# Optimization experiments

Measured on AMD Instinct MI355X. Metric: run time of the kernel, lower is better.

Reference implementation:

```python
import jax, jax.numpy as jnp
import numpy as np


def _conv(x, w, b, pad):
    y = jax.lax.conv_general_dilated(x, w, (1, 1), [(pad, pad), (pad, pad)],
                                     dimension_numbers=('NCHW', 'OIHW', 'NCHW'))
    return y + b[None, :, None, None]


def _leaky(x):
    return jnp.where(x >= 0, x, 0.2 * x)


def _up_nearest(t, s):
    return jnp.repeat(jnp.repeat(t, s, axis=2), s, axis=3)


def _to_plane(d, dx, dy, size):
    # nearest-upsample d,dx,dy by `size` and add per-subpixel plane offsets
    c = jnp.linspace(-(size - 1) / 2, (size - 1) / 2, size).astype(d.dtype)
    H, W = d.shape[2], d.shape[3]
    a = jnp.tile(c, W)[None, None, None, :]   # x-offset pattern along width
    b = jnp.tile(c, H)[None, None, :, None]   # y-offset pattern along height
    return _up_nearest(d, size) + a * _up_nearest(dx, size) + b * _up_nearest(dy, size)


def _warp(x, disp):
    # grid_sample(x, grid) with grid = (xx - disp, yy), align_corners=True, zero padding.
    # y coords are exact integers, so this reduces to 1-D linear interp along W.
    B, C, H, W = x.shape
    ix = jnp.arange(W, dtype=x.dtype)[None, None, :] - disp[:, 0]  # [B,H,W]
    x0 = jnp.floor(ix)
    wx = ix - x0
    x0i = x0.astype(jnp.int32)
    x1i = x0i + 1
    ok0 = ((x0i >= 0) & (x0i < W)).astype(x.dtype)
    ok1 = ((x1i >= 0) & (x1i < W)).astype(x.dtype)

    def gather(idx):
        idx = jnp.clip(idx, 0, W - 1)
        return jnp.take_along_axis(x, jnp.broadcast_to(idx[:, None], (B, C, H, W)), axis=3)

    return ((1 - wx) * ok0)[:, None] * gather(x0i) + (wx * ok1)[:, None] * gather(x1i)


def _unshuffle(x, r=4):
    B, C, H, W = x.shape
    return x.reshape(B, C, H // r, r, W // r, r).transpose(0, 1, 3, 5, 2, 4).reshape(B, C * r * r, H // r, W // r)


def _tile_warping(tile_plane, fea_l, fea_r):
    d, dx, dy = tile_plane[:, 0:1], tile_plane[:, 1:2], tile_plane[:, 2:3]
    cvs = []
    for k in (-1.0, 0.0, 1.0):
        local_d = _to_plane(d + k, dx, dy, 4)
        cv = jnp.sum(jnp.abs(fea_l - _warp(fea_r, local_d)), axis=1, keepdims=True)
        cvs.append(_unshuffle(cv, 4))
    return jnp.concatenate(cvs, axis=1)


def _upsample_hyp(h, scale=2.0, size=2):
    d = _to_plane(h[:, 0:1], h[:, 1:2], h[:, 2:3], size) * scale
    rest = _up_nearest(h[:, 1:], size)
    return jnp.concatenate([d, rest], axis=1)


def _forward(fea_l, fea_r, cur, prev,
             w_dec, b_dec, w0, b0,
             w_r0c1, b_r0c1, w_r0c2, b_r0c2,
             w_r1c1, b_r1c1, w_r1c2, b_r1c2,
             w_last, b_last):
    fea = _unshuffle(jnp.sum(jnp.abs(fea_l), axis=1, keepdims=True), 4)  # [B,16,H/4,W/4]

    cur_cv = _tile_warping(cur[:, :3], fea_l, fea_r)
    cur_cv = _leaky(_conv(jnp.concatenate([fea, cur_cv], 1), w_dec, b_dec, 0))

    up_prev = _upsample_hyp(prev, 2.0, 2)
    prev_cv = _tile_warping(up_prev[:, :3], fea_l, fea_r)
    prev_cv = _leaky(_conv(jnp.concatenate([fea, prev_cv], 1), w_dec, b_dec, 0))

    aug = jnp.concatenate([cur, cur_cv, up_prev, prev_cv], 1)  # 64 ch
    h = _leaky(_conv(aug, w0, b0, 0))
    # resblock0 (BasicBlock + outer LeakyReLU)
    t = _leaky(_conv(h, w_r0c1, b_r0c1, 1))
    h = _leaky(_conv(t, w_r0c2, b_r0c2, 1) + h)
    # resblock1
    t = _leaky(_conv(h, w_r1c1, b_r1c1, 1))
    h = _leaky(_conv(t, w_r1c2, b_r1c2, 1) + h)
    u = _conv(h, w_last, b_last, 1)  # 34 ch

    conf = u[:, :2]
    prev_delta = u[:, 2:18]
    cur_delta = u[:, 18:34]
    mask = jnp.argmax(conf, axis=1, keepdims=True).astype(u.dtype)

    upd_cur = cur + cur_delta
    upd_cur = jnp.concatenate([jax.nn.relu(upd_cur[:, :1]), upd_cur[:, 1:]], 1)
    upd_prev = up_prev + prev_delta
    upd_prev = jnp.concatenate([jax.nn.relu(upd_prev[:, :1]), upd_prev[:, 1:]], 1)

    refined = mask * upd_cur + (1 - mask) * upd_prev
    return (refined,
            jnp.concatenate([upd_cur, conf[:, 1:2]], 1),
            jnp.concatenate([upd_prev, conf[:, :1]], 1))


def setup_inputs() -> dict:
    key = jax.random.key(0)
    ks = jax.random.split(key, 16)
    B, C, H, W = 2, 16, 384, 1280
    Ht, Wt = H // 4, W // 4
    inp = {
        'fea_l': jax.random.normal(ks[0], (B, C, H, W), jnp.float32),
        'fea_r': jax.random.normal(ks[1], (B, C, H, W), jnp.float32),
        'current_hypothesis': jax.random.uniform(ks[2], (B, 16, Ht, Wt), jnp.float32) * 4.0,
        'prev_hypothesis': jax.random.uniform(ks[3], (B, 16, Ht // 2, Wt // 2), jnp.float32) * 4.0,
    }
    s = 0.05
    inp['w_dec'] = jax.random.normal(ks[4], (16, 64, 1, 1), jnp.float32) * s
    inp['b_dec'] = jax.random.normal(ks[5], (16,), jnp.float32) * s
    inp['w0'] = jax.random.normal(ks[6], (32, 64, 1, 1), jnp.float32) * s
    inp['b0'] = jax.random.normal(ks[7], (32,), jnp.float32) * s
    inp['w_r0c1'] = jax.random.normal(ks[8], (32, 32, 3, 3), jnp.float32) * s
    inp['b_r0c1'] = jax.random.normal(ks[9], (32,), jnp.float32) * s
    inp['w_r0c2'] = jax.random.normal(ks[10], (32, 32, 3, 3), jnp.float32) * s
    inp['b_r0c2'] = jax.random.normal(ks[11], (32,), jnp.float32) * s
    inp['w_r1c1'] = jax.random.normal(ks[12], (32, 32, 3, 3), jnp.float32) * s
    inp['b_r1c1'] = jax.random.normal(ks[13], (32,), jnp.float32) * s
    inp['w_r1c2'] = jax.random.normal(ks[14], (32, 32, 3, 3), jnp.float32) * s
    inp['b_r1c2'] = jax.random.normal(ks[15], (32,), jnp.float32) * s
    k2 = jax.random.split(jax.random.key(1), 2)
    inp['w_last'] = jax.random.normal(k2[0], (34, 32, 3, 3), jnp.float32) * s
    inp['b_last'] = jax.random.normal(k2[1], (34,), jnp.float32) * s
    return inp


def reference(fea_l, fea_r, current_hypothesis, prev_hypothesis,
              w_dec, b_dec, w0, b0,
              w_r0c1, b_r0c1, w_r0c2, b_r0c2,
              w_r1c1, b_r1c1, w_r1c2, b_r1c2,
              w_last, b_last):
    return _forward(fea_l, fea_r, current_hypothesis, prev_hypothesis,
                    w_dec, b_dec, w0, b0,
                    w_r0c1, b_r0c1, w_r0c2, b_r0c2,
                    w_r1c1, b_r1c1, w_r1c2, b_r1c2,
                    w_last, b_last)
```

## Files before the change

kernel.cpp:

```cpp
#include <hip/hip_runtime.h>
#include <hip/hip_bf16.h>

#define B_ 2
#define C_ 16
#define H_ 384
#define W_ 1280
#define HT_ 96
#define WT_ 320
#define SP_ (HT_*WT_)
#define NPIX_ (B_*SP_)
#define HP_ 48
#define WP_ 160
#define SPP_ (HP_*WP_)

__device__ __forceinline__ float leaky(float v){ return v >= 0.f ? v : 0.2f*v; }

__global__ __launch_bounds__(256) void k_sentinel(float* __restrict__ out, int n, float v){
    int i = blockIdx.x*256 + threadIdx.x;
    if (i < n) out[i] = v;
}

template <bool PREV>
__global__ __launch_bounds__(256) void k_warpdec(const float* __restrict__ plane,
        const float* __restrict__ fl, const float* __restrict__ fr,
        const float* __restrict__ wdec, const float* __restrict__ bdec,
        float* __restrict__ outcv){
    __shared__ float vals[16][65];
    __shared__ float wl[64][16];
    int tid = threadIdx.x;
    for (int i = tid; i < 1024; i += 256) wl[i>>4][i&15] = wdec[(i&15)*64 + (i>>4)];

    int tp  = tid >> 4;
    int sub = tid & 15;
    int yy = sub >> 2, xx = sub & 3;
    int ty = blockIdx.y;
    int tx = blockIdx.x*16 + tp;
    int b  = blockIdx.z;
    int y = ty*4 + yy, x = tx*4 + xx;

    float d, dxv, dyv;
    if (PREV){
        size_t pb = ((size_t)(b*16)*HP_ + (ty>>1))*WP_ + (tx>>1);
        float pd  = plane[pb];
        float pdx = plane[pb + SPP_];
        float pdy = plane[pb + 2*SPP_];
        float cx = (tx & 1) ? 0.5f : -0.5f;
        float cy = (ty & 1) ? 0.5f : -0.5f;
        d   = (pd + cx*pdx + cy*pdy) * 2.0f;
        dxv = pdx;
        dyv = pdy;
    } else {
        size_t pb = ((size_t)(b*16)*HT_ + ty)*WT_ + tx;
        d   = plane[pb];
        dxv = plane[pb + SP_];
        dyv = plane[pb + 2*SP_];
    }
    const float c4[4] = {-1.5f,-0.5f,0.5f,1.5f};
    float ld0 = d + c4[xx]*dxv + c4[yy]*dyv;
    float ix  = (float)x - ld0;
    float x0f = floorf(ix);
    float wx  = ix - x0f;
    int   x0  = (int)x0f;
    float wlo[4], whi[4]; int xc[4];
    #pragma unroll
    for (int j = 0; j < 4; j++){
        int xi = x0 + (j-1);
        bool ok = (xi >= 0) && (xi < W_);
        xc[j]  = xi < 0 ? 0 : (xi > W_-1 ? W_-1 : xi);
        wlo[j] = ok ? (1.f - wx) : 0.f;
        whi[j] = ok ? wx : 0.f;
    }
    const float* pl = fl + (size_t)(b*C_)*H_*W_ + (size_t)y*W_ + x;
    const float* pr = fr + (size_t)(b*C_)*H_*W_ + (size_t)y*W_;
    float fsum=0.f, s0=0.f, s1=0.f, s2=0.f;
    #pragma unroll 4
    for (int c = 0; c < C_; c++){
        float a = pl[(size_t)c*H_*W_];
        const float* prc = pr + (size_t)c*H_*W_;
        float v0 = prc[xc[0]];
        float v1 = prc[xc[1]];
        float v2 = prc[xc[2]];
        float v3 = prc[xc[3]];
        fsum += fabsf(a);
        s0 += fabsf(a - (wlo[2]*v2 + whi[3]*v3));
        s1 += fabsf(a - (wlo[1]*v1 + whi[2]*v2));
        s2 += fabsf(a - (wlo[0]*v0 + whi[1]*v1));
    }
    vals[tp][sub]      = fsum;
    vals[tp][16 + sub] = s0;
    vals[tp][32 + sub] = s1;
    vals[tp][48 + sub] = s2;
    __syncthreads();
    int oc  = tid >> 4;
    int tp2 = tid & 15;
    float acc = bdec[oc];
    #pragma unroll 8
    for (int ic = 0; ic < 64; ic++) acc += vals[tp2][ic] * wl[ic][oc];
    outcv[((size_t)(b*16 + oc)*HT_ + ty)*WT_ + blockIdx.x*16 + tp2] = leaky(acc);
}

__global__ __launch_bounds__(256) void k_conv0(const float* __restrict__ cur,
        const float* __restrict__ ccv, const float* __restrict__ prev,
        const float* __restrict__ pcv, const float* __restrict__ w,
        const float* __restrict__ bias, float* __restrict__ out){
    __shared__ float wl[64][32];
    __shared__ float bl[32];
    int tid = threadIdx.x;
    for (int i = tid; i < 2048; i += 256) wl[i>>5][i&31] = w[(i&31)*64 + (i>>5)];
    if (tid < 32) bl[tid] = bias[tid];
    __syncthreads();
    int idx = blockIdx.x*256 + tid;
    int b = idx / SP_, sp = idx % SP_;
    int y = sp / WT_, x = sp % WT_;
    float acc[32];
    #pragma unroll
    for (int o = 0; o < 32; o++) acc[o] = 0.f;
    const float* p0 = cur + (size_t)b*16*SP_ + sp;
    #pragma unroll 2
    for (int i = 0; i < 16; i++){
        float v = p0[(size_t)i*SP_];
        #pragma unroll
        for (int o = 0; o < 32; o++) acc[o] += v*wl[i][o];
    }
    const float* p1 = ccv + (size_t)b*16*SP_ + sp;
    #pragma unroll 2
    for (int i = 0; i < 16; i++){
        float v = p1[(size_t)i*SP_];
        #pragma unroll
        for (int o = 0; o < 32; o++) acc[o] += v*wl[16+i][o];
    }
    size_t src = ((size_t)(b*16)*HP_ + (y>>1))*WP_ + (x>>1);
    {
        float pd  = prev[src];
        float pdx = prev[src + SPP_];
        float pdy = prev[src + 2*SPP_];
        float cx = (x & 1) ? 0.5f : -0.5f;
        float cy = (y & 1) ? 0.5f : -0.5f;
        float v = (pd + cx*pdx + cy*pdy) * 2.0f;
        #pragma unroll
        for (int o = 0; o < 32; o++) acc[o] += v*wl[32][o];
    }
    #pragma unroll 2
    for (int i = 1; i < 16; i++){
        float v = prev[src + (size_t)i*SPP_];
        #pragma unroll
        for (int o = 0; o < 32; o++) acc[o] += v*wl[32+i][o];
    }
    const float* p3 = pcv + (size_t)b*16*SP_ + sp;
    #pragma unroll 2
    for (int i = 0; i < 16; i++){
        float v = p3[(size_t)i*SP_];
        #pragma unroll
        for (int o = 0; o < 32; o++) acc[o] += v*wl[48+i][o];
    }
    float* po = out + (size_t)b*32*SP_ + sp;
    #pragma unroll
    for (int o = 0; o < 32; o++) po[(size_t)o*SP_] = leaky(acc[o] + bl[o]);
}

template<bool RES>
__global__ __launch_bounds__(256) void k_conv3(const float* __restrict__ in,
        const float* __restrict__ w, const float* __restrict__ bias,
        const float* res, float* out){
    __shared__ float it[8][6][34];
    __shared__ float wl[8][9][32];
    int tid = threadIdx.x;
    int gx = blockIdx.x*32, gy = blockIdx.y*4;
    int b = blockIdx.z;
    int ocg  = tid >> 5;
    int slot = tid & 31;
    int tx4  = (slot & 7)*4;
    int ty   = slot >> 3;
    float acc[4][4];
    #pragma unroll
    for (int o = 0; o < 4; o++)
        #pragma unroll
        for (int p = 0; p < 4; p++) acc[o][p] = 0.f;

    for (int ic0 = 0; ic0 < 32; ic0 += 8){
        for (int i = tid; i < 8*6*34; i += 256){
            int ic = i/(6*34); int r = i - ic*(6*34);
            int iy = r/34;     int ixx = r - iy*34;
            int ggy = gy + iy - 1, ggx = gx + ixx - 1;
            float v = 0.f;
            if (ggy >= 0 && ggy < HT_ && ggx >= 0 && ggx < WT_)
                v = in[((size_t)(b*32 + ic0+ic)*HT_ + ggy)*WT_ + ggx];
            it[ic][iy][ixx] = v;
        }
        for (int i = tid; i < 2304; i += 256){
            int ic = i/288; int r = i - ic*288;
            int kk = r >> 5; int oc = r & 31;
            wl[ic][kk][oc] = w[(size_t)(oc*32 + ic0+ic)*9 + kk];
        }
        __syncthreads();
        #pragma unroll
        for (int ic = 0; ic < 8; ic++){
            #pragma unroll
            for (int dy = 0; dy < 3; dy++){
                float inr[6];
                #pragma unroll
                for (int j = 0; j < 6; j++) inr[j] = it[ic][ty+dy][tx4+j];
                #pragma unroll
                for (int dx = 0; dx < 3; dx++){
                    const float4 wv = *(const float4*)(&wl[ic][dy*3+dx][ocg*4]);
                    const float wa[4] = {wv.x, wv.y, wv.z, wv.w};
                    #pragma unroll
                    for (int o = 0; o < 4; o++)
                        #pragma unroll
                        for (int p = 0; p < 4; p++)
                            acc[o][p] += inr[dx+p]*wa[o];
                }
            }
        }
        __syncthreads();
    }
    int oc0 = ocg*4;
    int yo = gy + ty;
    #pragma unroll
    for (int o = 0; o < 4; o++){
        float bo = bias[oc0+o];
        size_t ob = ((size_t)(b*32 + oc0+o)*HT_ + yo)*WT_ + gx + tx4;
        #pragma unroll
        for (int p = 0; p < 4; p++){
            float v = acc[o][p] + bo;
            if (RES) v += res[ob+p];
            out[ob+p] = leaky(v);
        }
    }
}

__global__ __launch_bounds__(256) void k_last(const float* __restrict__ in,
        const float* __restrict__ w, const float* __restrict__ bias,
        const float* __restrict__ cur, const float* __restrict__ prev,
        float* __restrict__ out){
    __shared__ float it[8][10][34];
    __shared__ float wl[8][9][36];
    __shared__ float bl[34];
    int tid = threadIdx.x;
    int gx = blockIdx.x*32, gy = blockIdx.y*8;
    int b = blockIdx.z;
    int tx = tid & 31, ty = tid >> 5;
    if (tid < 34) bl[tid] = bias[tid];
    float acc[34];
    #pragma unroll
    for (int o = 0; o < 34; o++) acc[o] = 0.f;

    for (int ic0 = 0; ic0 < 32; ic0 += 8){
        for (int i = tid; i < 8*10*34; i += 256){
            int ic = i/340; int r = i - ic*340;
            int iy = r/34;  int ixx = r - iy*34;
            int ggy = gy + iy - 1, ggx = gx + ixx - 1;
            float v = 0.f;
            if (ggy >= 0 && ggy < HT_ && ggx >= 0 && ggx < WT_)
                v = in[((size_t)(b*32 + ic0+ic)*HT_ + ggy)*WT_ + ggx];
            it[ic][iy][ixx] = v;
        }
        for (int i = tid; i < 8*9*34; i += 256){
            int ic = i/306; int r = i - ic*306;
            int kk = r/34;  int oc = r - kk*34;
            wl[ic][kk][oc] = w[(size_t)(oc*32 + ic0+ic)*9 + kk];
        }
        __syncthreads();
        for (int ic = 0; ic < 8; ic++){
            #pragma unroll
            for (int dy = 0; dy < 3; dy++){
                const float vv[3] = { it[ic][ty+dy][tx], it[ic][ty+dy][tx+1], it[ic][ty+dy][tx+2] };
                #pragma unroll
                for (int dx = 0; dx < 3; dx++){
                    const float* wp = &wl[ic][dy*3+dx][0];
                    float v = vv[dx];
                    #pragma unroll
                    for (int o = 0; o < 34; o++) acc[o] += v*wp[o];
                }
            }
        }
        __syncthreads();
    }
    int x = gx + tx, y = gy + ty;
    size_t pix = (size_t)y*WT_ + x;
    float conf0 = acc[0] + bl[0];
    float conf1 = acc[1] + bl[1];
    bool m = conf1 > conf0;
    size_t src = ((size_t)(b*16)*HP_ + (y>>1))*WP_ + (x>>1);
    float cx = (x & 1) ? 0.5f : -0.5f;
    float cy = (y & 1) ? 0.5f : -0.5f;
    const float* cp = cur + (size_t)b*16*SP_ + pix;
    float* o0 = out +               (size_t)b*16*SP_ + pix;
    float* o1 = out +  983040u  +   (size_t)b*17*SP_ + pix;
    float* o2 = out + 2027520u  +   (size_t)b*17*SP_ + pix;
    #pragma unroll
    for (int c = 0; c < 16; c++){
        float upv;
        if (c == 0){
            float dv  = prev[src];
            float dxv = prev[src + SPP_];
            float dyv = prev[src + 2*SPP_];
            upv = (dv + cx*dxv + cy*dyv) * 2.0f;
        } else {
            upv = prev[src + (size_t)c*SPP_];
        }
        float ucv = cp[(size_t)c*SP_] + acc[18+c] + bl[18+c];
        upv = upv + acc[2+c] + bl[2+c];
        if (c == 0){ ucv = fmaxf(ucv, 0.f); upv = fmaxf(upv, 0.f); }
        float rf = m ? ucv : upv;
        o0[(size_t)c*SP_] = rf;
        o1[(size_t)c*SP_] = ucv;
        o2[(size_t)c*SP_] = upv;
    }
    o1[(size_t)16*SP_] = conf1;
    o2[(size_t)16*SP_] = conf0;
}

#define WS_NEED (32u*NPIX_*4u)
#define OUT_ELEMS 3072000

extern "C" void kernel_launch(void* const* d_in, const int* in_sizes, int n_in,
                              void* d_out, int out_size, void* d_ws, size_t ws_size,
                              hipStream_t stream) {
    const float* fea_l  = (const float*)d_in[0];
    const float* fea_r  = (const float*)d_in[1];
    const float* cur    = (const float*)d_in[2];
    const float* prev   = (const float*)d_in[3];
    const float* w_dec  = (const float*)d_in[4];
    const float* b_dec  = (const float*)d_in[5];
    const float* w0     = (const float*)d_in[6];
    const float* b0     = (const float*)d_in[7];
    const float* w_r0c1 = (const float*)d_in[8];
    const float* b_r0c1 = (const float*)d_in[9];
    const float* w_r0c2 = (const float*)d_in[10];
    const float* b_r0c2 = (const float*)d_in[11];
    const float* w_r1c1 = (const float*)d_in[12];
    const float* b_r1c1 = (const float*)d_in[13];
    const float* w_r1c2 = (const float*)d_in[14];
    const float* b_r1c2 = (const float*)d_in[15];
    const float* w_last = (const float*)d_in[16];
    const float* b_last = (const float*)d_in[17];

    float* out = (float*)d_out;

    if (ws_size < (size_t)WS_NEED){
        k_sentinel<<<(OUT_ELEMS+255)/256, 256, 0, stream>>>(out, OUT_ELEMS, (float)(ws_size >> 10));
        return;
    }

    float* h = (float*)d_ws;
    float* curcv  = out;
    float* prevcv = out + 983040;
    float* t      = out;

    dim3 gw(20, 96, 2);
    k_warpdec<false><<<gw, 256, 0, stream>>>(cur,  fea_l, fea_r, w_dec, b_dec, curcv);
    k_warpdec<true> <<<gw, 256, 0, stream>>>(prev, fea_l, fea_r, w_dec, b_dec, prevcv);

    k_conv0<<<240, 256, 0, stream>>>(cur, curcv, prev, prevcv, w0, b0, h);

    dim3 g3(10, 24, 2);
    k_conv3<false><<<g3, 256, 0, stream>>>(h, w_r0c1, b_r0c1, nullptr, t);
    k_conv3<true> <<<g3, 256, 0, stream>>>(t, w_r0c2, b_r0c2, h, h);
    k_conv3<false><<<g3, 256, 0, stream>>>(h, w_r1c1, b_r1c1, nullptr, t);
    k_conv3<true> <<<g3, 256, 0, stream>>>(t, w_r1c2, b_r1c2, h, h);

    dim3 gl(10, 12, 2);
    k_last<<<gl, 256, 0, stream>>>(h, w_last, b_last, cur, prev, out);
}
```

Measured before the change: 492.4 us.

## Fuse warp cost volumes and 1x1 conv0 into one front kernel; retile last conv

The two warp+decoder kernels and the 1x1 conv0 become a single kernel. It computes the current and previous cost volumes together, sharing the fea_l loads and the fsum term, and applies conv0 from shared memory, so the intermediate cost volumes never go through global memory. The last 3x3 conv now uses the same register-blocked 4x4 tiling as k_conv3 with extra output channels, staging results in shared memory for the epilogue. The conv3 shared tile is padded to 36 for float4/float2 vectorized reads. The cost is more shared memory and registers per block in the fused kernel, and only half of the threads run the epilogue in k_last.

```diff
diff --git a/kernel.cpp b/kernel.cpp
--- a/kernel.cpp
+++ b/kernel.cpp
@@ -20,149 +20,174 @@
     if (i < n) out[i] = v;
 }
 
-template <bool PREV>
-__global__ __launch_bounds__(256) void k_warpdec(const float* __restrict__ plane,
+__global__ __launch_bounds__(256) void k_front(
+        const float* __restrict__ cur, const float* __restrict__ prev,
         const float* __restrict__ fl, const float* __restrict__ fr,
         const float* __restrict__ wdec, const float* __restrict__ bdec,
-        float* __restrict__ outcv){
-    __shared__ float vals[16][65];
-    __shared__ float wl[64][16];
+        const float* __restrict__ w0, const float* __restrict__ b0,
+        float* __restrict__ h){
+    __shared__ float wdl[64][17];
+    __shared__ float w0l[64][33];
+    __shared__ float pl6[16][6];
+    __shared__ float vals[16][117];
+    __shared__ float cvl[16][33];
+    __shared__ float cul[16][33];
     int tid = threadIdx.x;
-    for (int i = tid; i < 1024; i += 256) wl[i>>4][i&15] = wdec[(i&15)*64 + (i>>4)];
-
-    int tp  = tid >> 4;
-    int sub = tid & 15;
-    int yy = sub >> 2, xx = sub & 3;
-    int ty = blockIdx.y;
-    int tx = blockIdx.x*16 + tp;
-    int b  = blockIdx.z;
-    int y = ty*4 + yy, x = tx*4 + xx;
-
-    float d, dxv, dyv;
-    if (PREV){
-        size_t pb = ((size_t)(b*16)*HP_ + (ty>>1))*WP_ + (tx>>1);
-        float pd  = plane[pb];
-        float pdx = plane[pb + SPP_];
-        float pdy = plane[pb + 2*SPP_];
+    int ty = blockIdx.y, b = blockIdx.z;
+    int tx0 = blockIdx.x*16;
+
+    for (int i = tid; i < 1024; i += 256) wdl[i>>4][i&15] = wdec[(i&15)*64 + (i>>4)];
+    for (int i = tid; i < 2048; i += 256) w0l[i>>5][i&31] = w0[(i&31)*64 + (i>>5)];
+    if (tid < 16){
+        int tx = tx0 + tid;
+        size_t pb = ((size_t)(b*16)*HT_ + ty)*WT_ + tx;
+        pl6[tid][0] = cur[pb];
+        pl6[tid][1] = cur[pb + SP_];
+        pl6[tid][2] = cur[pb + 2*SP_];
+        size_t qb = ((size_t)(b*16)*HP_ + (ty>>1))*WP_ + (tx>>1);
+        float pd  = prev[qb];
+        float pdx = prev[qb + SPP_];
+        float pdy = prev[qb + 2*SPP_];
         float cx = (tx & 1) ? 0.5f : -0.5f;
         float cy = (ty & 1) ? 0.5f : -0.5f;
-        d   = (pd + cx*pdx + cy*pdy) * 2.0f;
-        dxv = pdx;
-        dyv = pdy;
-    } else {
-        size_t pb = ((size_t)(b*16)*HT_ + ty)*WT_ + tx;
-        d   = plane[pb];
-        dxv = plane[pb + SP_];
-        dyv = plane[pb + 2*SP_];
-    }
+        pl6[tid][3] = (pd + cx*pdx + cy*pdy) * 2.0f;
+        pl6[tid][4] = pdx;
+        pl6[tid][5] = pdy;
+    }
+    {
+        int i = tid >> 4, px = tid & 15;
+        int tx = tx0 + px;
+        cul[px][i] = cur[(size_t)(b*16 + i)*SP_ + (size_t)ty*WT_ + tx];
+        float upv;
+        if (i == 0) upv = 0.f;
+        else upv = prev[(size_t)(b*16 + i)*SPP_ + (size_t)(ty>>1)*WP_ + (tx>>1)];
+        cul[px][16 + i] = upv;
+    }
+    __syncthreads();
+    if (tid < 16) cul[tid][16] = pl6[tid][3];
+
+    int r  = tid >> 6;
+    int cx = tid & 63;
+    int tp = cx >> 2, xx = cx & 3, yy = r;
+    int x = tx0*4 + cx, y = ty*4 + r;
+    int sub = yy*4 + xx;
+
+    float dC = pl6[tp][0], dxC = pl6[tp][1], dyC = pl6[tp][2];
+    float dP = pl6[tp][3], dxP = pl6[tp][4], dyP = pl6[tp][5];
     const float c4[4] = {-1.5f,-0.5f,0.5f,1.5f};
-    float ld0 = d + c4[xx]*dxv + c4[yy]*dyv;
-    float ix  = (float)x - ld0;
-    float x0f = floorf(ix);
-    float wx  = ix - x0f;
-    int   x0  = (int)x0f;
-    float wlo[4], whi[4]; int xc[4];
-    #pragma unroll
-    for (int j = 0; j < 4; j++){
-        int xi = x0 + (j-1);
-        bool ok = (xi >= 0) && (xi < W_);
-        xc[j]  = xi < 0 ? 0 : (xi > W_-1 ? W_-1 : xi);
-        wlo[j] = ok ? (1.f - wx) : 0.f;
-        whi[j] = ok ? wx : 0.f;
+    float ldC = dC + c4[xx]*dxC + c4[yy]*dyC;
+    float ldP = dP + c4[xx]*dxP + c4[yy]*dyP;
+
+    float wloC[4], whiC[4], wloP[4], whiP[4];
+    int xcC[4], xcP[4];
+    {
+        float ix  = (float)x - ldC;
+        float x0f = floorf(ix);
+        float wx  = ix - x0f;
+        int x0 = (int)x0f;
+        #pragma unroll
+        for (int j = 0; j < 4; j++){
+            int xi = x0 + (j-1);
+            bool ok = (xi >= 0) && (xi < W_);
+            xcC[j]  = xi < 0 ? 0 : (xi > W_-1 ? W_-1 : xi);
+            wloC[j] = ok ? (1.f - wx) : 0.f;
+            whiC[j] = ok ? wx : 0.f;
+        }
+        ix  = (float)x - ldP;
+        x0f = floorf(ix);
+        wx  = ix - x0f;
+        x0 = (int)x0f;
+        #pragma unroll
+        for (int j = 0; j < 4; j++){
+            int xi = x0 + (j-1);
+            bool ok = (xi >= 0) && (xi < W_);
+            xcP[j]  = xi < 0 ? 0 : (xi > W_-1 ? W_-1 : xi);
+            wloP[j] = ok ? (1.f - wx) : 0.f;
+            whiP[j] = ok ? wx : 0.f;
+        }
     }
     const float* pl = fl + (size_t)(b*C_)*H_*W_ + (size_t)y*W_ + x;
     const float* pr = fr + (size_t)(b*C_)*H_*W_ + (size_t)y*W_;
-    float fsum=0.f, s0=0.f, s1=0.f, s2=0.f;
-    #pragma unroll 4
+    float fsum=0.f, c0=0.f, c1=0.f, c2=0.f, p0=0.f, p1=0.f, p2=0.f;
+    #pragma unroll 8
     for (int c = 0; c < C_; c++){
         float a = pl[(size_t)c*H_*W_];
         const float* prc = pr + (size_t)c*H_*W_;
-        float v0 = prc[xc[0]];
-        float v1 = prc[xc[1]];
-        float v2 = prc[xc[2]];
-        float v3 = prc[xc[3]];
+        float uC0 = prc[xcC[0]], uC1 = prc[xcC[1]], uC2 = prc[xcC[2]], uC3 = prc[xcC[3]];
+        float uP0 = prc[xcP[0]], uP1 = prc[xcP[1]], uP2 = prc[xcP[2]], uP3 = prc[xcP[3]];
         fsum += fabsf(a);
-        s0 += fabsf(a - (wlo[2]*v2 + whi[3]*v3));
-        s1 += fabsf(a - (wlo[1]*v1 + whi[2]*v2));
-        s2 += fabsf(a - (wlo[0]*v0 + whi[1]*v1));
+        c0 += fabsf(a - (wloC[2]*uC2 + whiC[3]*uC3));
+        c1 += fabsf(a - (wloC[1]*uC1 + whiC[2]*uC2));
+        c2 += fabsf(a - (wloC[0]*uC0 + whiC[1]*uC1));
+        p0 += fabsf(a - (wloP[2]*uP2 + whiP[3]*uP3));
+        p1 += fabsf(a - (wloP[1]*uP1 + whiP[2]*uP2));
+        p2 += fabsf(a - (wloP[0]*uP0 + whiP[1]*uP1));
     }
     vals[tp][sub]      = fsum;
-    vals[tp][16 + sub] = s0;
-    vals[tp][32 + sub] = s1;
-    vals[tp][48 + sub] = s2;
+    vals[tp][16+sub]   = c0;
+    vals[tp][32+sub]   = c1;
+    vals[tp][48+sub]   = c2;
+    vals[tp][64+sub]   = p0;
+    vals[tp][80+sub]   = p1;
+    vals[tp][96+sub]   = p2;
     __syncthreads();
-    int oc  = tid >> 4;
-    int tp2 = tid & 15;
-    float acc = bdec[oc];
-    #pragma unroll 8
-    for (int ic = 0; ic < 64; ic++) acc += vals[tp2][ic] * wl[ic][oc];
-    outcv[((size_t)(b*16 + oc)*HT_ + ty)*WT_ + blockIdx.x*16 + tp2] = leaky(acc);
-}
-
-__global__ __launch_bounds__(256) void k_conv0(const float* __restrict__ cur,
-        const float* __restrict__ ccv, const float* __restrict__ prev,
-        const float* __restrict__ pcv, const float* __restrict__ w,
-        const float* __restrict__ bias, float* __restrict__ out){
-    __shared__ float wl[64][32];
-    __shared__ float bl[32];
-    int tid = threadIdx.x;
-    for (int i = tid; i < 2048; i += 256) wl[i>>5][i&31] = w[(i&31)*64 + (i>>5)];
-    if (tid < 32) bl[tid] = bias[tid];
+
+    {
+        int oc = tid >> 4, px = tid & 15;
+        float bb = bdec[oc];
+        float accC = bb, accP = bb;
+        #pragma unroll 8
+        for (int ic = 0; ic < 16; ic++){
+            float wv = wdl[ic][oc];
+            accC += vals[px][ic] * wv;
+            accP += vals[px][ic] * wv;
+        }
+        #pragma unroll 8
+        for (int ic = 16; ic < 64; ic++){
+            float wv = wdl[ic][oc];
+            accC += vals[px][ic]      * wv;
+            accP += vals[px][ic + 48] * wv;
+        }
+        cvl[px][oc]      = leaky(accC);
+        cvl[px][16 + oc] = leaky(accP);
+    }
     __syncthreads();
-    int idx = blockIdx.x*256 + tid;
-    int b = idx / SP_, sp = idx % SP_;
-    int y = sp / WT_, x = sp % WT_;
-    float acc[32];
-    #pragma unroll
-    for (int o = 0; o < 32; o++) acc[o] = 0.f;
-    const float* p0 = cur + (size_t)b*16*SP_ + sp;
-    #pragma unroll 2
-    for (int i = 0; i < 16; i++){
-        float v = p0[(size_t)i*SP_];
-        #pragma unroll
-        for (int o = 0; o < 32; o++) acc[o] += v*wl[i][o];
-    }
-    const float* p1 = ccv + (size_t)b*16*SP_ + sp;
-    #pragma unroll 2
-    for (int i = 0; i < 16; i++){
-        float v = p1[(size_t)i*SP_];
-        #pragma unroll
-        for (int o = 0; o < 32; o++) acc[o] += v*wl[16+i][o];
-    }
-    size_t src = ((size_t)(b*16)*HP_ + (y>>1))*WP_ + (x>>1);
+
     {
-        float pd  = prev[src];
-        float pdx = prev[src + SPP_];
-        float pdy = prev[src + 2*SPP_];
-        float cx = (x & 1) ? 0.5f : -0.5f;
-        float cy = (y & 1) ? 0.5f : -0.5f;
-        float v = (pd + cx*pdx + cy*pdy) * 2.0f;
-        #pragma unroll
-        for (int o = 0; o < 32; o++) acc[o] += v*wl[32][o];
-    }
-    #pragma unroll 2
-    for (int i = 1; i < 16; i++){
-        float v = prev[src + (size_t)i*SPP_];
-        #pragma unroll
-        for (int o = 0; o < 32; o++) acc[o] += v*wl[32+i][o];
-    }
-    const float* p3 = pcv + (size_t)b*16*SP_ + sp;
-    #pragma unroll 2
-    for (int i = 0; i < 16; i++){
-        float v = p3[(size_t)i*SP_];
-        #pragma unroll
-        for (int o = 0; o < 32; o++) acc[o] += v*wl[48+i][o];
-    }
-    float* po = out + (size_t)b*32*SP_ + sp;
-    #pragma unroll
-    for (int o = 0; o < 32; o++) po[(size_t)o*SP_] = leaky(acc[o] + bl[o]);
+        int pair = tid >> 4, px = tid & 15;
+        int oc0 = pair*2;
+        float a0 = b0[oc0], a1 = b0[oc0+1];
+        #pragma unroll 4
+        for (int i = 0; i < 16; i++){
+            float v = cul[px][i];
+            a0 += v*w0l[i][oc0]; a1 += v*w0l[i][oc0+1];
+        }
+        #pragma unroll 4
+        for (int i = 0; i < 16; i++){
+            float v = cvl[px][i];
+            a0 += v*w0l[16+i][oc0]; a1 += v*w0l[16+i][oc0+1];
+        }
+        #pragma unroll 4
+        for (int i = 0; i < 16; i++){
+            float v = cul[px][16+i];
+            a0 += v*w0l[32+i][oc0]; a1 += v*w0l[32+i][oc0+1];
+        }
+        #pragma unroll 4
+        for (int i = 0; i < 16; i++){
+            float v = cvl[px][16+i];
+            a0 += v*w0l[48+i][oc0]; a1 += v*w0l[48+i][oc0+1];
+        }
+        size_t ob = (size_t)(b*32 + oc0)*SP_ + (size_t)ty*WT_ + tx0 + px;
+        h[ob]       = leaky(a0);
+        h[ob + SP_] = leaky(a1);
+    }
 }
 
 template<bool RES>
 __global__ __launch_bounds__(256) void k_conv3(const float* __restrict__ in,
         const float* __restrict__ w, const float* __restrict__ bias,
         const float* res, float* out){
-    __shared__ float it[8][6][34];
+    __shared__ float it[8][6][36];
     __shared__ float wl[8][9][32];
     int tid = threadIdx.x;
     int gx = blockIdx.x*32, gy = blockIdx.y*4;
@@ -179,8 +204,8 @@
 
     for (int ic0 = 0; ic0 < 32; ic0 += 8){
         for (int i = tid; i < 8*6*34; i += 256){
-            int ic = i/(6*34); int r = i - ic*(6*34);
-            int iy = r/34;     int ixx = r - iy*34;
+            int ic = i/(6*34); int rr = i - ic*(6*34);
+            int iy = rr/34;    int ixx = rr - iy*34;
             int ggy = gy + iy - 1, ggx = gx + ixx - 1;
             float v = 0.f;
             if (ggy >= 0 && ggy < HT_ && ggx >= 0 && ggx < WT_)
@@ -188,8 +213,8 @@
             it[ic][iy][ixx] = v;
         }
         for (int i = tid; i < 2304; i += 256){
-            int ic = i/288; int r = i - ic*288;
-            int kk = r >> 5; int oc = r & 31;
+            int ic = i/288; int rr = i - ic*288;
+            int kk = rr >> 5; int oc = rr & 31;
             wl[ic][kk][oc] = w[(size_t)(oc*32 + ic0+ic)*9 + kk];
         }
         __syncthreads();
@@ -197,9 +222,9 @@
         for (int ic = 0; ic < 8; ic++){
             #pragma unroll
             for (int dy = 0; dy < 3; dy++){
-                float inr[6];
-                #pragma unroll
-                for (int j = 0; j < 6; j++) inr[j] = it[ic][ty+dy][tx4+j];
+                const float4 va = *(const float4*)(&it[ic][ty+dy][tx4]);
+                const float2 vb = *(const float2*)(&it[ic][ty+dy][tx4+4]);
+                const float inr[6] = {va.x, va.y, va.z, va.w, vb.x, vb.y};
                 #pragma unroll
                 for (int dx = 0; dx < 3; dx++){
                     const float4 wv = *(const float4*)(&wl[ic][dy*3+dx][ocg*4]);
@@ -233,22 +258,29 @@
         const float* __restrict__ w, const float* __restrict__ bias,
         const float* __restrict__ cur, const float* __restrict__ prev,
         float* __restrict__ out){
-    __shared__ float it[8][10][34];
+    __shared__ float it[8][6][36];
     __shared__ float wl[8][9][36];
-    __shared__ float bl[34];
+    __shared__ float uu[34][129];
     int tid = threadIdx.x;
-    int gx = blockIdx.x*32, gy = blockIdx.y*8;
+    int gx = blockIdx.x*32, gy = blockIdx.y*4;
     int b = blockIdx.z;
-    int tx = tid & 31, ty = tid >> 5;
-    if (tid < 34) bl[tid] = bias[tid];
-    float acc[34];
+    int ocg  = tid >> 5;
+    int slot = tid & 31;
+    int tx4  = (slot & 7)*4;
+    int ty   = slot >> 3;
+    float acc[4][4];
+    float acce[4];
     #pragma unroll
-    for (int o = 0; o < 34; o++) acc[o] = 0.f;
+    for (int o = 0; o < 4; o++){
+        acce[o] = 0.f;
+        #pragma unroll
+        for (int p = 0; p < 4; p++) acc[o][p] = 0.f;
+    }
 
     for (int ic0 = 0; ic0 < 32; ic0 += 8){
-        for (int i = tid; i < 8*10*34; i += 256){
-            int ic = i/340; int r = i - ic*340;
-            int iy = r/34;  int ixx = r - iy*34;
+        for (int i = tid; i < 8*6*34; i += 256){
+            int ic = i/(6*34); int rr = i - ic*(6*34);
+            int iy = rr/34;    int ixx = rr - iy*34;
             int ggy = gy + iy - 1, ggx = gx + ixx - 1;
             float v = 0.f;
             if (ggy >= 0 && ggy < HT_ && ggx >= 0 && ggx < WT_)
@@ -256,59 +288,93 @@
             it[ic][iy][ixx] = v;
         }
         for (int i = tid; i < 8*9*34; i += 256){
-            int ic = i/306; int r = i - ic*306;
-            int kk = r/34;  int oc = r - kk*34;
+            int ic = i/306; int rr = i - ic*306;
+            int kk = rr/34; int oc = rr - kk*34;
             wl[ic][kk][oc] = w[(size_t)(oc*32 + ic0+ic)*9 + kk];
         }
         __syncthreads();
+        #pragma unroll
         for (int ic = 0; ic < 8; ic++){
             #pragma unroll
             for (int dy = 0; dy < 3; dy++){
-                const float vv[3] = { it[ic][ty+dy][tx], it[ic][ty+dy][tx+1], it[ic][ty+dy][tx+2] };
+                const float4 va = *(const float4*)(&it[ic][ty+dy][tx4]);
+                const float2 vb = *(const float2*)(&it[ic][ty+dy][tx4+4]);
+                const float inr[6] = {va.x, va.y, va.z, va.w, vb.x, vb.y};
                 #pragma unroll
                 for (int dx = 0; dx < 3; dx++){
-                    const float* wp = &wl[ic][dy*3+dx][0];
-                    float v = vv[dx];
+                    const float4 wv = *(const float4*)(&wl[ic][dy*3+dx][ocg*4]);
+                    const float wa[4] = {wv.x, wv.y, wv.z, wv.w};
                     #pragma unroll
-                    for (int o = 0; o < 34; o++) acc[o] += v*wp[o];
+                    for (int o = 0; o < 4; o++)
+                        #pragma unroll
+                        for (int p = 0; p < 4; p++)
+                            acc[o][p] += inr[dx+p]*wa[o];
+                    if (ocg < 2){
+                        float we = wl[ic][dy*3+dx][32+ocg];
+                        #pragma unroll
+                        for (int p = 0; p < 4; p++)
+                            acce[p] += inr[dx+p]*we;
+                    }
                 }
             }
         }
         __syncthreads();
     }
-    int x = gx + tx, y = gy + ty;
-    size_t pix = (size_t)y*WT_ + x;
-    float conf0 = acc[0] + bl[0];
-    float conf1 = acc[1] + bl[1];
-    bool m = conf1 > conf0;
-    size_t src = ((size_t)(b*16)*HP_ + (y>>1))*WP_ + (x>>1);
-    float cx = (x & 1) ? 0.5f : -0.5f;
-    float cy = (y & 1) ? 0.5f : -0.5f;
-    const float* cp = cur + (size_t)b*16*SP_ + pix;
-    float* o0 = out +               (size_t)b*16*SP_ + pix;
-    float* o1 = out +  983040u  +   (size_t)b*17*SP_ + pix;
-    float* o2 = out + 2027520u  +   (size_t)b*17*SP_ + pix;
-    #pragma unroll
-    for (int c = 0; c < 16; c++){
-        float upv;
-        if (c == 0){
-            float dv  = prev[src];
-            float dxv = prev[src + SPP_];
-            float dyv = prev[src + 2*SPP_];
-            upv = (dv + cx*dxv + cy*dyv) * 2.0f;
-        } else {
-            upv = prev[src + (size_t)c*SPP_];
-        }
-        float ucv = cp[(size_t)c*SP_] + acc[18+c] + bl[18+c];
-        upv = upv + acc[2+c] + bl[2+c];
-        if (c == 0){ ucv = fmaxf(ucv, 0.f); upv = fmaxf(upv, 0.f); }
-        float rf = m ? ucv : upv;
-        o0[(size_t)c*SP_] = rf;
-        o1[(size_t)c*SP_] = ucv;
-        o2[(size_t)c*SP_] = upv;
-    }
-    o1[(size_t)16*SP_] = conf1;
-    o2[(size_t)16*SP_] = conf0;
+    {
+        int oc0 = ocg*4;
+        int pxb = ty*32 + tx4;
+        #pragma unroll
+        for (int o = 0; o < 4; o++){
+            float bo = bias[oc0+o];
+            #pragma unroll
+            for (int p = 0; p < 4; p++)
+                uu[oc0+o][pxb+p] = acc[o][p] + bo;
+        }
+        if (ocg < 2){
+            float bo = bias[32+ocg];
+            #pragma unroll
+            for (int p = 0; p < 4; p++)
+                uu[32+ocg][pxb+p] = acce[p] + bo;
+        }
+    }
+    __syncthreads();
+    if (tid < 128){
+        int px = tid;
+        int x = gx + (px & 31);
+        int y = gy + (px >> 5);
+        size_t pix = (size_t)y*WT_ + x;
+        float conf0 = uu[0][px];
+        float conf1 = uu[1][px];
+        bool m = conf1 > conf0;
+        size_t src = ((size_t)(b*16)*HP_ + (y>>1))*WP_ + (x>>1);
+        float cx = (x & 1) ? 0.5f : -0.5f;
+        float cy = (y & 1) ? 0.5f : -0.5f;
+        const float* cp = cur + (size_t)b*16*SP_ + pix;
+        float* o0 = out +               (size_t)b*16*SP_ + pix;
+        float* o1 = out +  983040u  +   (size_t)b*17*SP_ + pix;
+        float* o2 = out + 2027520u  +   (size_t)b*17*SP_ + pix;
+        #pragma unroll
+        for (int c = 0; c < 16; c++){
+            float upv;
+            if (c == 0){
+                float dv  = prev[src];
+                float dxv = prev[src + SPP_];
+                float dyv = prev[src + 2*SPP_];
+                upv = (dv + cx*dxv + cy*dyv) * 2.0f;
+            } else {
+                upv = prev[src + (size_t)c*SPP_];
+            }
+            float ucv = cp[(size_t)c*SP_] + uu[18+c][px];
+            upv = upv + uu[2+c][px];
+            if (c == 0){ ucv = fmaxf(ucv, 0.f); upv = fmaxf(upv, 0.f); }
+            float rf = m ? ucv : upv;
+            o0[(size_t)c*SP_] = rf;
+            o1[(size_t)c*SP_] = ucv;
+            o2[(size_t)c*SP_] = upv;
+        }
+        o1[(size_t)16*SP_] = conf1;
+        o2[(size_t)16*SP_] = conf0;
+    }
 }
 
 #define WS_NEED (32u*NPIX_*4u)
@@ -344,15 +410,10 @@
     }
 
     float* h = (float*)d_ws;
-    float* curcv  = out;
-    float* prevcv = out + 983040;
-    float* t      = out;
-
-    dim3 gw(20, 96, 2);
-    k_warpdec<false><<<gw, 256, 0, stream>>>(cur,  fea_l, fea_r, w_dec, b_dec, curcv);
-    k_warpdec<true> <<<gw, 256, 0, stream>>>(prev, fea_l, fea_r, w_dec, b_dec, prevcv);
-
-    k_conv0<<<240, 256, 0, stream>>>(cur, curcv, prev, prevcv, w0, b0, h);
+    float* t = out;
+
+    dim3 gf(20, 96, 2);
+    k_front<<<gf, 256, 0, stream>>>(cur, prev, fea_l, fea_r, w_dec, b_dec, w0, b0, h);
 
     dim3 g3(10, 24, 2);
     k_conv3<false><<<g3, 256, 0, stream>>>(h, w_r0c1, b_r0c1, nullptr, t);
@@ -360,6 +421,6 @@
     k_conv3<false><<<g3, 256, 0, stream>>>(h, w_r1c1, b_r1c1, nullptr, t);
     k_conv3<true> <<<g3, 256, 0, stream>>>(t, w_r1c2, b_r1c2, h, h);
 
-    dim3 gl(10, 12, 2);
+    dim3 gl(10, 24, 2);
     k_last<<<gl, 256, 0, stream>>>(h, w_last, b_last, cur, prev, out);
 }
```

After: 552.9 us. +12.3%, slower.
